# Optimization experiments

Measured on AMD Instinct MI355X. Metric: run time of the kernel, lower is better.

The kernel has to match this reference:

```python
import jax, jax.numpy as jnp
import numpy as np

N_GRAPHS = 256
BN_EPS = 1e-5

def gcn_conv(x, row, col, W, b, n):
    # PyG GCNConv: add self-loops, symmetric deg^-1/2 normalization, scatter-add at col.
    deg = jnp.zeros((n,), x.dtype).at[col].add(1.0) + 1.0  # +1 for self-loop
    dinv = jax.lax.rsqrt(deg)
    xw = x @ W                                             # [N, H]
    msg = (dinv[row] * dinv[col])[:, None] * xw[row]       # [E, H] gathered messages
    agg = jnp.zeros_like(xw).at[col].add(msg)              # scatter-add to targets
    agg = agg + (dinv * dinv)[:, None] * xw                # self-loop contribution
    return agg + b

def batch_norm(x, gamma, beta):
    # BatchNorm1d over the node dimension (training-mode batch statistics)
    mu = jnp.mean(x, axis=0)
    var = jnp.var(x, axis=0)
    return (x - mu) * jax.lax.rsqrt(var + BN_EPS) * gamma + beta

def setup_inputs():
    key = jax.random.key(0)
    ks = jax.random.split(key, 8)
    N, F, H, C, E = 50000, 128, 128, 3, 1_600_000
    x = jax.random.normal(ks[0], (N, F), jnp.float32)
    edge_index = jax.random.randint(ks[1], (2, E), 0, N)
    batch = jnp.sort(jax.random.randint(ks[2], (N,), 0, N_GRAPHS))
    s = lambda k, sh, fan: jax.random.normal(k, sh, jnp.float32) / np.sqrt(fan).astype(np.float32)
    return {
        "x": x, "edge_index": edge_index, "batch": batch,
        "W1": s(ks[3], (F, H), F), "b1": jnp.zeros((H,), jnp.float32),
        "gamma1": jnp.ones((H,), jnp.float32), "beta1": jnp.zeros((H,), jnp.float32),
        "W2": s(ks[4], (H, H), H), "b2": jnp.zeros((H,), jnp.float32),
        "gamma2": jnp.ones((H,), jnp.float32), "beta2": jnp.zeros((H,), jnp.float32),
        "Wc": s(ks[5], (3 * H, C), 3 * H), "bc": jnp.zeros((C,), jnp.float32),
    }

def reference(x, edge_index, batch, W1, b1, gamma1, beta1, W2, b2, gamma2, beta2, Wc, bc):
    n = x.shape[0]
    row, col = edge_index[0], edge_index[1]
    h = jax.nn.relu(batch_norm(gcn_conv(x, row, col, W1, b1, n), gamma1, beta1))
    # dropout is identity in eval mode
    h = jax.nn.relu(batch_norm(gcn_conv(h, row, col, W2, b2, n), gamma2, beta2))
    cnt = jax.ops.segment_sum(jnp.ones((n,), h.dtype), batch, num_segments=N_GRAPHS)
    hsum = jax.ops.segment_sum(h, batch, num_segments=N_GRAPHS)
    hmean = hsum / jnp.maximum(cnt, 1.0)[:, None]
    hmax = jax.ops.segment_max(h, batch, num_segments=N_GRAPHS)
    hmax = jnp.where(cnt[:, None] > 0, hmax, 0.0)  # guard empty graphs
    g = jnp.concatenate([hmean, hmax, hsum], axis=1)  # [G, 3H]
    return g @ Wc + bc
```

## Files before the change

kernel.cpp:

```cpp
#include <hip/hip_runtime.h>

#define HF 128
#define TILE 128
#define CAP2 6144
#define NFINE_MAX 512
#define SORT_CHUNK 2048
#define BN_EPS 1e-5f
#define SMEM_FUSED 22528

__device__ __forceinline__ unsigned short f2bf(float f) {
    unsigned u = __float_as_uint(f);
    unsigned rounding = 0x7FFF + ((u >> 16) & 1);
    return (unsigned short)((u + rounding) >> 16);
}
__device__ __forceinline__ float bf2f(unsigned short u) {
    return __uint_as_float(((unsigned)u) << 16);
}
__device__ __forceinline__ unsigned packbf(float lo, float hi) {
    return ((unsigned)f2bf(hi) << 16) | (unsigned)f2bf(lo);
}

__device__ __forceinline__ void bucket_sort_block(char* smem, int bid,
                                                  const int* __restrict__ row,
                                                  const int* __restrict__ col,
                                                  unsigned* __restrict__ buckets,
                                                  int* __restrict__ cursor,
                                                  int E, int nfine) {
    unsigned* staged = (unsigned*)smem;
    unsigned short* sbkt = (unsigned short*)(smem + 8192);
    int* hist  = (int*)(smem + 12288);
    int* lbase = (int*)(smem + 14336);
    int* gbase = (int*)(smem + 16384);
    int* lofs  = (int*)(smem + 18432);
    int* s     = (int*)(smem + 20480);
    int t = threadIdx.x;
    for (int i = t; i < NFINE_MAX; i += 256) { hist[i] = 0; lofs[i] = 0; }
    __syncthreads();
    int e0 = bid * SORT_CHUNK + t * 8;
    int cc[8], rr[8], pg[8];
    unsigned pk[8];
    if (e0 + 8 <= E) {
        int4 c0 = *reinterpret_cast<const int4*>(col + e0);
        int4 c1 = *reinterpret_cast<const int4*>(col + e0 + 4);
        int4 r0 = *reinterpret_cast<const int4*>(row + e0);
        int4 r1 = *reinterpret_cast<const int4*>(row + e0 + 4);
        cc[0]=c0.x; cc[1]=c0.y; cc[2]=c0.z; cc[3]=c0.w;
        cc[4]=c1.x; cc[5]=c1.y; cc[6]=c1.z; cc[7]=c1.w;
        rr[0]=r0.x; rr[1]=r0.y; rr[2]=r0.z; rr[3]=r0.w;
        rr[4]=r1.x; rr[5]=r1.y; rr[6]=r1.z; rr[7]=r1.w;
    } else {
        #pragma unroll
        for (int i = 0; i < 8; ++i) {
            int e = e0 + i;
            cc[i] = (e < E) ? col[e] : -1;
            rr[i] = (e < E) ? row[e] : 0;
        }
    }
    #pragma unroll
    for (int i = 0; i < 8; ++i) {
        if (cc[i] >= 0) {
            int b = cc[i] >> 7;
            pg[i] = b;
            pk[i] = ((unsigned)(cc[i] & 127) << 17) | (unsigned)rr[i];
            atomicAdd(&hist[b], 1);
        } else {
            pg[i] = -1;
        }
    }
    __syncthreads();
    s[t] = hist[t];
    s[t + 256] = hist[t + 256];
    for (int o = 1; o < 512; o <<= 1) {
        __syncthreads();
        int idx = (t + 1) * (o << 1) - 1;
        if (idx < 512) s[idx] += s[idx - o];
    }
    __syncthreads();
    if (t == 0) s[511] = 0;
    for (int o = 256; o >= 1; o >>= 1) {
        __syncthreads();
        int idx = (t + 1) * (o << 1) - 1;
        if (idx < 512) { int tmp = s[idx - o]; s[idx - o] = s[idx]; s[idx] += tmp; }
    }
    __syncthreads();
    lbase[t] = s[t];
    lbase[t + 256] = s[t + 256];
    for (int b = t; b < nfine; b += 256) {
        int cnt = hist[b];
        gbase[b] = cnt ? atomicAdd(&cursor[b * 16], cnt) : 0;
    }
    __syncthreads();
    #pragma unroll
    for (int i = 0; i < 8; ++i) {
        if (pg[i] >= 0) {
            int pos = lbase[pg[i]] + atomicAdd(&lofs[pg[i]], 1);
            staged[pos] = pk[i];
            sbkt[pos] = (unsigned short)pg[i];
        }
    }
    __syncthreads();
    int n = min(SORT_CHUNK, E - bid * SORT_CHUNK);
    for (int i = t; i < n; i += 256) {
        int b = sbkt[i];
        int pos = gbase[b] + (i - lbase[b]);
        if (pos < CAP2) buckets[(size_t)b * CAP2 + pos] = staged[i];
    }
}

__device__ __forceinline__ void gemm_block32(char* smem, int bid,
                                             const float* __restrict__ X,
                                             const float* __restrict__ W,
                                             unsigned short* __restrict__ Y, int N) {
    float (*xst)[36] = (float(*)[36])smem;
    int t = threadIdx.x;
    int row0 = bid * 32;
    {
        int f = t & 127;
        for (int r = (t >> 7); r < 32; r += 2) {
            int rr = row0 + r;
            xst[f][r] = (rr < N) ? X[(size_t)rr * HF + f] : 0.0f;
        }
    }
    __syncthreads();
    int cg = t & 31;
    int rg = t >> 5;
    int r0 = rg * 4;
    float acc[4][4] = {};
    const float4* Wv = reinterpret_cast<const float4*>(W);
    #pragma unroll 4
    for (int f = 0; f < HF; ++f) {
        float4 w = Wv[f * 32 + cg];
        float4 xv = *reinterpret_cast<const float4*>(&xst[f][r0]);
        float xr[4] = {xv.x, xv.y, xv.z, xv.w};
        #pragma unroll
        for (int i = 0; i < 4; ++i) {
            acc[i][0] += xr[i] * w.x;
            acc[i][1] += xr[i] * w.y;
            acc[i][2] += xr[i] * w.z;
            acc[i][3] += xr[i] * w.w;
        }
    }
    #pragma unroll
    for (int i = 0; i < 4; ++i) {
        int rr = row0 + r0 + i;
        if (rr < N) {
            ushort4 o;
            o.x = f2bf(acc[i][0]);
            o.y = f2bf(acc[i][1]);
            o.z = f2bf(acc[i][2]);
            o.w = f2bf(acc[i][3]);
            *reinterpret_cast<ushort4*>(&Y[(size_t)rr * HF + cg * 4]) = o;
        }
    }
}

__global__ __launch_bounds__(256) void sort_gemm1(const int* __restrict__ row,
                                                  const int* __restrict__ col,
                                                  unsigned* __restrict__ buckets,
                                                  int* __restrict__ cursor,
                                                  int E, int nfine, int nsort,
                                                  const float* __restrict__ x,
                                                  const float* __restrict__ W1,
                                                  unsigned short* __restrict__ A,
                                                  int N) {
    __shared__ __align__(16) char smem[SMEM_FUSED];
    if (blockIdx.x < nsort)
        bucket_sort_block(smem, blockIdx.x, row, col, buckets, cursor, E, nfine);
    else
        gemm_block32(smem, blockIdx.x - nsort, x, W1, A, N);
}

__global__ __launch_bounds__(256) void gemm_rt(const unsigned short* __restrict__ Xh,
                                               const float* __restrict__ W,
                                               unsigned short* __restrict__ Y,
                                               const float* __restrict__ scale,
                                               const float* __restrict__ shift,
                                               const float* __restrict__ rowscale,
                                               int N) {
    __shared__ float xst[HF][68];
    int t = threadIdx.x;
    int row0 = blockIdx.x * 64;
    {
        int f = t & 127;
        float sc = scale[f];
        float sh = shift[f];
        for (int r = (t >> 7); r < 64; r += 2) {
            int rr = row0 + r;
            float v = 0.0f;
            if (rr < N) {
                v = bf2f(Xh[(size_t)rr * HF + f]);
                v = fmaxf(v * sc + sh, 0.0f);
            }
            xst[f][r] = v;
        }
    }
    __syncthreads();
    int cg = t & 31;
    int rg = t >> 5;
    int r0 = rg * 8;
    float acc[8][4] = {};
    const float4* Wv = reinterpret_cast<const float4*>(W);
    #pragma unroll 2
    for (int f = 0; f < HF; ++f) {
        float4 w = Wv[f * 32 + cg];
        float4 x0 = *reinterpret_cast<const float4*>(&xst[f][r0]);
        float4 x1 = *reinterpret_cast<const float4*>(&xst[f][r0 + 4]);
        float xr[8] = {x0.x, x0.y, x0.z, x0.w, x1.x, x1.y, x1.z, x1.w};
        #pragma unroll
        for (int i = 0; i < 8; ++i) {
            acc[i][0] += xr[i] * w.x;
            acc[i][1] += xr[i] * w.y;
            acc[i][2] += xr[i] * w.z;
            acc[i][3] += xr[i] * w.w;
        }
    }
    #pragma unroll
    for (int i = 0; i < 8; ++i) {
        int rr = row0 + r0 + i;
        if (rr < N) {
            float rs = rowscale[rr];
            ushort4 o;
            o.x = f2bf(acc[i][0] * rs);
            o.y = f2bf(acc[i][1] * rs);
            o.z = f2bf(acc[i][2] * rs);
            o.w = f2bf(acc[i][3] * rs);
            *reinterpret_cast<ushort4*>(&Y[(size_t)rr * HF + cg * 4]) = o;
        }
    }
}

__global__ __launch_bounds__(256) void tile_place2(const unsigned* __restrict__ buckets,
                                                   const int* __restrict__ cursor,
                                                   int* __restrict__ rowptr,
                                                   float* __restrict__ dinv,
                                                   int* __restrict__ srow,
                                                   unsigned short* __restrict__ A,
                                                   const int* __restrict__ batch,
                                                   int* __restrict__ gstart,
                                                   int N, int NG, int nfine) {
    int b = blockIdx.x;
    int t = threadIdx.x;
    if (b < 2 && t < 129) {
        int g = b * 129 + t;
        if (g <= NG) {
            int lo = 0, hi = N;
            while (lo < hi) {
                int mid = (lo + hi) >> 1;
                if (batch[mid] < g) lo = mid + 1; else hi = mid;
            }
            gstart[g] = lo;
        }
    }
    __shared__ int h[TILE], loc[TILE], cur[TILE];
    __shared__ float dloc[TILE];
    __shared__ int red[256];
    __shared__ int stage[CAP2];
    int part = 0;
    for (int i = t; i < b; i += 256) part += min(cursor[i * 16], CAP2);
    red[t] = part;
    if (t < TILE) h[t] = 0;
    __syncthreads();
    for (int o = 128; o > 0; o >>= 1) {
        if (t < o) red[t] += red[t + o];
        __syncthreads();
    }
    int base = red[0];
    int sz = min(cursor[b * 16], CAP2);
    const unsigned* bk = buckets + (size_t)b * CAP2;
    for (int i = t; i < sz; i += 256) atomicAdd(&h[bk[i] >> 17], 1);
    __syncthreads();
    if (t < TILE) loc[t] = h[t];
    __syncthreads();
    for (int o = 1; o < TILE; o <<= 1) {
        int v = (t < TILE && t >= o) ? loc[t - o] : 0;
        __syncthreads();
        if (t < TILE) loc[t] += v;
        __syncthreads();
    }
    int c0 = b * TILE;
    int ncols = min(TILE, N - c0);
    if (t < TILE) {
        int c = c0 + t;
        int excl = loc[t] - h[t];
        float dc = rsqrtf((float)h[t] + 1.0f);
        if (c < N) {
            rowptr[c] = base + excl;
            dinv[c] = dc;
        }
        dloc[t] = dc;
        cur[t] = excl;
    }
    if (b == nfine - 1 && t == 0) rowptr[N] = base + sz;
    __syncthreads();
    for (int i = t; i < sz; i += 256) {
        unsigned p = bk[i];
        int pos = atomicAdd(&cur[p >> 17], 1);
        if (pos < CAP2) stage[pos] = (int)(p & 0x1FFFFu);
    }
    __syncthreads();
    for (int i = t; i < sz; i += 256) srow[base + i] = stage[i];
    const unsigned M = 0xffff0000u;
    for (int i = t; i < ncols * 16; i += 256) {
        int nl = i >> 4, j = i & 15;
        float dc = dloc[nl];
        unsigned short* ap = A + (size_t)(c0 + nl) * HF + j * 8;
        uint4 u = *reinterpret_cast<const uint4*>(ap);
        uint4 o;
        o.x = packbf(__uint_as_float(u.x << 16) * dc, __uint_as_float(u.x & M) * dc);
        o.y = packbf(__uint_as_float(u.y << 16) * dc, __uint_as_float(u.y & M) * dc);
        o.z = packbf(__uint_as_float(u.z << 16) * dc, __uint_as_float(u.z & M) * dc);
        o.w = packbf(__uint_as_float(u.w << 16) * dc, __uint_as_float(u.w & M) * dc);
        *reinterpret_cast<uint4*>(ap) = o;
    }
}

__global__ __launch_bounds__(256) void gather_conv(const int* __restrict__ rowptr,
                                                   const int* __restrict__ srow,
                                                   const float* __restrict__ dinv,
                                                   const unsigned short* __restrict__ XW,
                                                   const float* __restrict__ b,
                                                   unsigned short* __restrict__ OUT,
                                                   float* __restrict__ psum,
                                                   float* __restrict__ psq, int N) {
    int blk = blockIdx.x;
    int c = blk * 16 + (threadIdx.x >> 4);
    int j = threadIdx.x & 15;
    bool valid = (c < N);
    const unsigned M = 0xffff0000u;
    float o[8];
    if (valid) {
        int e = rowptr[c], end = rowptr[c + 1];
        float acc[8] = {0.f, 0.f, 0.f, 0.f, 0.f, 0.f, 0.f, 0.f};
        for (; e + 3 < end; e += 4) {
            int r0 = srow[e], r1 = srow[e + 1], r2 = srow[e + 2], r3 = srow[e + 3];
            uint4 u0 = *reinterpret_cast<const uint4*>(XW + (size_t)r0 * HF + j * 8);
            uint4 u1 = *reinterpret_cast<const uint4*>(XW + (size_t)r1 * HF + j * 8);
            uint4 u2 = *reinterpret_cast<const uint4*>(XW + (size_t)r2 * HF + j * 8);
            uint4 u3 = *reinterpret_cast<const uint4*>(XW + (size_t)r3 * HF + j * 8);
            acc[0] += (__uint_as_float(u0.x << 16) + __uint_as_float(u1.x << 16))
                    + (__uint_as_float(u2.x << 16) + __uint_as_float(u3.x << 16));
            acc[1] += (__uint_as_float(u0.x & M) + __uint_as_float(u1.x & M))
                    + (__uint_as_float(u2.x & M) + __uint_as_float(u3.x & M));
            acc[2] += (__uint_as_float(u0.y << 16) + __uint_as_float(u1.y << 16))
                    + (__uint_as_float(u2.y << 16) + __uint_as_float(u3.y << 16));
            acc[3] += (__uint_as_float(u0.y & M) + __uint_as_float(u1.y & M))
                    + (__uint_as_float(u2.y & M) + __uint_as_float(u3.y & M));
            acc[4] += (__uint_as_float(u0.z << 16) + __uint_as_float(u1.z << 16))
                    + (__uint_as_float(u2.z << 16) + __uint_as_float(u3.z << 16));
            acc[5] += (__uint_as_float(u0.z & M) + __uint_as_float(u1.z & M))
                    + (__uint_as_float(u2.z & M) + __uint_as_float(u3.z & M));
            acc[6] += (__uint_as_float(u0.w << 16) + __uint_as_float(u1.w << 16))
                    + (__uint_as_float(u2.w << 16) + __uint_as_float(u3.w << 16));
            acc[7] += (__uint_as_float(u0.w & M) + __uint_as_float(u1.w & M))
                    + (__uint_as_float(u2.w & M) + __uint_as_float(u3.w & M));
        }
        for (; e < end; ++e) {
            int r0 = srow[e];
            uint4 u0 = *reinterpret_cast<const uint4*>(XW + (size_t)r0 * HF + j * 8);
            acc[0] += __uint_as_float(u0.x << 16);
            acc[1] += __uint_as_float(u0.x & M);
            acc[2] += __uint_as_float(u0.y << 16);
            acc[3] += __uint_as_float(u0.y & M);
            acc[4] += __uint_as_float(u0.z << 16);
            acc[5] += __uint_as_float(u0.z & M);
            acc[6] += __uint_as_float(u0.w << 16);
            acc[7] += __uint_as_float(u0.w & M);
        }
        float dc = dinv[c];
        uint4 xv = *reinterpret_cast<const uint4*>(XW + (size_t)c * HF + j * 8);
        acc[0] += __uint_as_float(xv.x << 16);
        acc[1] += __uint_as_float(xv.x & M);
        acc[2] += __uint_as_float(xv.y << 16);
        acc[3] += __uint_as_float(xv.y & M);
        acc[4] += __uint_as_float(xv.z << 16);
        acc[5] += __uint_as_float(xv.z & M);
        acc[6] += __uint_as_float(xv.w << 16);
        acc[7] += __uint_as_float(xv.w & M);
        float4 b0 = *reinterpret_cast<const float4*>(b + j * 8);
        float4 b1 = *reinterpret_cast<const float4*>(b + j * 8 + 4);
        o[0] = dc * acc[0] + b0.x;
        o[1] = dc * acc[1] + b0.y;
        o[2] = dc * acc[2] + b0.z;
        o[3] = dc * acc[3] + b0.w;
        o[4] = dc * acc[4] + b1.x;
        o[5] = dc * acc[5] + b1.y;
        o[6] = dc * acc[6] + b1.z;
        o[7] = dc * acc[7] + b1.w;
        uint4 ov;
        ov.x = packbf(o[0], o[1]);
        ov.y = packbf(o[2], o[3]);
        ov.z = packbf(o[4], o[5]);
        ov.w = packbf(o[6], o[7]);
        *reinterpret_cast<uint4*>(OUT + (size_t)c * HF + j * 8) = ov;
    } else {
        #pragma unroll
        for (int k = 0; k < 8; ++k) o[k] = 0.f;
    }
    __shared__ float sval[16][HF + 4];
    int r = threadIdx.x >> 4;
    *reinterpret_cast<float4*>(&sval[r][j * 8]) = make_float4(o[0], o[1], o[2], o[3]);
    *reinterpret_cast<float4*>(&sval[r][j * 8 + 4]) = make_float4(o[4], o[5], o[6], o[7]);
    __syncthreads();
    if (threadIdx.x < HF) {
        float s = 0.f, sq = 0.f;
        #pragma unroll
        for (int rr = 0; rr < 16; ++rr) {
            float v = sval[rr][threadIdx.x];
            s += v;
            sq += v * v;
        }
        psum[(size_t)blk * HF + threadIdx.x] = s;
        psq[(size_t)blk * HF + threadIdx.x] = sq;
    }
}

__global__ __launch_bounds__(256) void bn_reduce(const float* __restrict__ psum,
                                                 const float* __restrict__ psq,
                                                 const float* __restrict__ gamma,
                                                 const float* __restrict__ beta,
                                                 float* __restrict__ scale,
                                                 float* __restrict__ shift,
                                                 int nblk, int N) {
    int f = blockIdx.x;
    int t = threadIdx.x;
    float s = 0.f, sq = 0.f;
    for (int i = t; i < nblk; i += 256) {
        s += psum[(size_t)i * HF + f];
        sq += psq[(size_t)i * HF + f];
    }
    __shared__ float ls[256], lq[256];
    ls[t] = s; lq[t] = sq;
    __syncthreads();
    for (int o = 128; o > 0; o >>= 1) {
        if (t < o) { ls[t] += ls[t + o]; lq[t] += lq[t + o]; }
        __syncthreads();
    }
    if (t == 0) {
        float invn = 1.0f / (float)N;
        float mu = ls[0] * invn;
        float var = lq[0] * invn - mu * mu;
        float sc = gamma[f] * rsqrtf(var + BN_EPS);
        scale[f] = sc;
        shift[f] = beta[f] - mu * sc;
    }
}

__global__ __launch_bounds__(256) void pool_classify(const unsigned short* __restrict__ Bh,
                                                     const int* __restrict__ gstart,
                                                     const float* __restrict__ scale,
                                                     const float* __restrict__ shift,
                                                     const float* __restrict__ Wc,
                                                     const float* __restrict__ bc,
                                                     float* __restrict__ out) {
    int g = blockIdx.x;
    int t = threadIdx.x & 127;
    int half = threadIdx.x >> 7;
    int s0 = gstart[g], s1 = gstart[g + 1];
    float sc = scale[t], sh = shift[t];
    float sum = 0.f, mx = 0.f;
    for (int n = s0 + half; n < s1; n += 2) {
        float v = fmaxf(bf2f(Bh[(size_t)n * HF + t]) * sc + sh, 0.0f);
        sum += v;
        mx = fmaxf(mx, v);
    }
    __shared__ float shsum[2][HF], shmax[2][HF];
    __shared__ float red[3][HF];
    shsum[half][t] = sum;
    shmax[half][t] = mx;
    __syncthreads();
    if (half == 0) {
        sum += shsum[1][t];
        mx = fmaxf(mx, shmax[1][t]);
        float cntf = (float)(s1 - s0);
        float mean = sum / fmaxf(cntf, 1.0f);
        red[0][t] = mean * Wc[t * 3 + 0] + mx * Wc[(HF + t) * 3 + 0] + sum * Wc[(2 * HF + t) * 3 + 0];
        red[1][t] = mean * Wc[t * 3 + 1] + mx * Wc[(HF + t) * 3 + 1] + sum * Wc[(2 * HF + t) * 3 + 1];
        red[2][t] = mean * Wc[t * 3 + 2] + mx * Wc[(HF + t) * 3 + 2] + sum * Wc[(2 * HF + t) * 3 + 2];
    }
    __syncthreads();
    for (int o = 64; o > 0; o >>= 1) {
        if (half == 0 && t < o) {
            red[0][t] += red[0][t + o];
            red[1][t] += red[1][t + o];
            red[2][t] += red[2][t + o];
        }
        __syncthreads();
    }
    if (threadIdx.x < 3) out[g * 3 + threadIdx.x] = red[threadIdx.x][0] + bc[threadIdx.x];
}

extern "C" void kernel_launch(void* const* d_in, const int* in_sizes, int n_in,
                              void* d_out, int out_size, void* d_ws, size_t ws_size,
                              hipStream_t stream) {
    const float* x    = (const float*)d_in[0];
    const int*   ei   = (const int*)d_in[1];
    const int*   batch= (const int*)d_in[2];
    const float* W1   = (const float*)d_in[3];
    const float* b1   = (const float*)d_in[4];
    const float* g1   = (const float*)d_in[5];
    const float* be1  = (const float*)d_in[6];
    const float* W2   = (const float*)d_in[7];
    const float* b2   = (const float*)d_in[8];
    const float* g2   = (const float*)d_in[9];
    const float* be2  = (const float*)d_in[10];
    const float* Wc   = (const float*)d_in[11];
    const float* bc   = (const float*)d_in[12];
    float* out = (float*)d_out;

    const int N = in_sizes[0] / HF;
    const int E = in_sizes[1] / 2;
    const int NG = 256;
    const int* row = ei;
    const int* col = ei + E;
    const int total = N * HF;
    const int nfine = (N + TILE - 1) / TILE;
    const int nblkGa = (N + 15) / 16;

    char* w = (char*)d_ws;
    size_t off = 0;
    auto alloc = [&](size_t bytes) -> void* {
        void* p = w + off;
        off += (bytes + 255) & ~(size_t)255;
        return p;
    };
    int*            cursor    = (int*)alloc((size_t)nfine * 16 * 4);
    float*          dinv      = (float*)alloc((size_t)N * 4);
    int*            rowptr    = (int*)alloc(((size_t)N + 1) * 4);
    int*            gstart    = (int*)alloc((NG + 1) * 4);
    int*            srow      = (int*)alloc((size_t)E * 4);
    float*          psum      = (float*)alloc((size_t)nblkGa * HF * 4);
    float*          psq       = (float*)alloc((size_t)nblkGa * HF * 4);
    float*          scale     = (float*)alloc(HF * 4);
    float*          shift     = (float*)alloc(HF * 4);
    unsigned short* A         = (unsigned short*)alloc((size_t)total * 2);
    unsigned short* B         = (unsigned short*)alloc((size_t)total * 2);
    unsigned*       buckets   = (unsigned*)B;

    const int T256 = 256;
    int gridGemm64 = (N + 63) / 64;
    int gridGemm32 = (N + 31) / 32;
    int nsort      = (E + SORT_CHUNK - 1) / SORT_CHUNK;

    hipMemsetAsync(cursor, 0, (size_t)nfine * 16 * 4, stream);
    sort_gemm1<<<nsort + gridGemm32, T256, 0, stream>>>(row, col, buckets, cursor,
                                                        E, nfine, nsort, x, W1, A, N);
    tile_place2<<<nfine, T256, 0, stream>>>(buckets, cursor, rowptr, dinv, srow, A,
                                            batch, gstart, N, NG, nfine);

    gather_conv<<<nblkGa, T256, 0, stream>>>(rowptr, srow, dinv, A, b1, B, psum, psq, N);
    bn_reduce<<<HF, 256, 0, stream>>>(psum, psq, g1, be1, scale, shift, nblkGa, N);

    gemm_rt<<<gridGemm64, T256, 0, stream>>>(B, W2, A, scale, shift, dinv, N);
    gather_conv<<<nblkGa, T256, 0, stream>>>(rowptr, srow, dinv, A, b2, B, psum, psq, N);
    bn_reduce<<<HF, 256, 0, stream>>>(psum, psq, g2, be2, scale, shift, nblkGa, N);

    pool_classify<<<NG, 256, 0, stream>>>(B, gstart, scale, shift, Wc, bc, out);
}
```

Measured before the change: 292.8 us.

## Double sort chunk and first-GEMM row tile in fused sort/GEMM kernel

Each bucket-sort block now processes 4096 edges with strided loops that re-read col/row from global memory instead of holding 8 edges per thread in registers. Fewer blocks mean fewer global cursor atomics and longer contiguous runs per bucket. The first GEMM now computes 64 rows per block with 8x4 accumulators per thread, reusing each W load across more rows. Shared memory grows to about 34 KB and register use rises, which may reduce occupancy, and col is now read twice per edge.

```diff
diff --git a/kernel.cpp b/kernel.cpp
--- a/kernel.cpp
+++ b/kernel.cpp
@@ -4,9 +4,9 @@
 #define TILE 128
 #define CAP2 6144
 #define NFINE_MAX 512
-#define SORT_CHUNK 2048
+#define SORT_CHUNK 4096
 #define BN_EPS 1e-5f
-#define SMEM_FUSED 22528
+#define SMEM_BYTES 34816
 
 __device__ __forceinline__ unsigned short f2bf(float f) {
     unsigned u = __float_as_uint(f);
@@ -27,45 +27,20 @@
                                                   int* __restrict__ cursor,
                                                   int E, int nfine) {
     unsigned* staged = (unsigned*)smem;
-    unsigned short* sbkt = (unsigned short*)(smem + 8192);
-    int* hist  = (int*)(smem + 12288);
-    int* lbase = (int*)(smem + 14336);
-    int* gbase = (int*)(smem + 16384);
-    int* lofs  = (int*)(smem + 18432);
-    int* s     = (int*)(smem + 20480);
+    unsigned short* sbkt = (unsigned short*)(smem + 16384);
+    int* hist  = (int*)(smem + 24576);
+    int* lbase = (int*)(smem + 26624);
+    int* gbase = (int*)(smem + 28672);
+    int* lofs  = (int*)(smem + 30720);
+    int* s     = (int*)(smem + 32768);
     int t = threadIdx.x;
     for (int i = t; i < NFINE_MAX; i += 256) { hist[i] = 0; lofs[i] = 0; }
     __syncthreads();
-    int e0 = bid * SORT_CHUNK + t * 8;
-    int cc[8], rr[8], pg[8];
-    unsigned pk[8];
-    if (e0 + 8 <= E) {
-        int4 c0 = *reinterpret_cast<const int4*>(col + e0);
-        int4 c1 = *reinterpret_cast<const int4*>(col + e0 + 4);
-        int4 r0 = *reinterpret_cast<const int4*>(row + e0);
-        int4 r1 = *reinterpret_cast<const int4*>(row + e0 + 4);
-        cc[0]=c0.x; cc[1]=c0.y; cc[2]=c0.z; cc[3]=c0.w;
-        cc[4]=c1.x; cc[5]=c1.y; cc[6]=c1.z; cc[7]=c1.w;
-        rr[0]=r0.x; rr[1]=r0.y; rr[2]=r0.z; rr[3]=r0.w;
-        rr[4]=r1.x; rr[5]=r1.y; rr[6]=r1.z; rr[7]=r1.w;
-    } else {
-        #pragma unroll
-        for (int i = 0; i < 8; ++i) {
-            int e = e0 + i;
-            cc[i] = (e < E) ? col[e] : -1;
-            rr[i] = (e < E) ? row[e] : 0;
-        }
-    }
-    #pragma unroll
-    for (int i = 0; i < 8; ++i) {
-        if (cc[i] >= 0) {
-            int b = cc[i] >> 7;
-            pg[i] = b;
-            pk[i] = ((unsigned)(cc[i] & 127) << 17) | (unsigned)rr[i];
-            atomicAdd(&hist[b], 1);
-        } else {
-            pg[i] = -1;
-        }
+    int e0 = bid * SORT_CHUNK;
+    int n = min(SORT_CHUNK, E - e0);
+    for (int i = t; i < n; i += 256) {
+        int c = col[e0 + i];
+        atomicAdd(&hist[c >> 7], 1);
     }
     __syncthreads();
     s[t] = hist[t];
@@ -90,16 +65,15 @@
         gbase[b] = cnt ? atomicAdd(&cursor[b * 16], cnt) : 0;
     }
     __syncthreads();
-    #pragma unroll
-    for (int i = 0; i < 8; ++i) {
-        if (pg[i] >= 0) {
-            int pos = lbase[pg[i]] + atomicAdd(&lofs[pg[i]], 1);
-            staged[pos] = pk[i];
-            sbkt[pos] = (unsigned short)pg[i];
-        }
-    }
-    __syncthreads();
-    int n = min(SORT_CHUNK, E - bid * SORT_CHUNK);
+    for (int i = t; i < n; i += 256) {
+        int c = col[e0 + i];
+        int r = row[e0 + i];
+        int b = c >> 7;
+        int pos = lbase[b] + atomicAdd(&lofs[b], 1);
+        staged[pos] = ((unsigned)(c & 127) << 17) | (unsigned)r;
+        sbkt[pos] = (unsigned short)b;
+    }
+    __syncthreads();
     for (int i = t; i < n; i += 256) {
         int b = sbkt[i];
         int pos = gbase[b] + (i - lbase[b]);
@@ -107,16 +81,16 @@
     }
 }
 
-__device__ __forceinline__ void gemm_block32(char* smem, int bid,
+__device__ __forceinline__ void gemm_block64(char* smem, int bid,
                                              const float* __restrict__ X,
                                              const float* __restrict__ W,
                                              unsigned short* __restrict__ Y, int N) {
-    float (*xst)[36] = (float(*)[36])smem;
+    float (*xst)[68] = (float(*)[68])smem;
     int t = threadIdx.x;
-    int row0 = bid * 32;
+    int row0 = bid * 64;
     {
         int f = t & 127;
-        for (int r = (t >> 7); r < 32; r += 2) {
+        for (int r = (t >> 7); r < 64; r += 2) {
             int rr = row0 + r;
             xst[f][r] = (rr < N) ? X[(size_t)rr * HF + f] : 0.0f;
         }
@@ -124,16 +98,17 @@
     __syncthreads();
     int cg = t & 31;
     int rg = t >> 5;
-    int r0 = rg * 4;
-    float acc[4][4] = {};
+    int r0 = rg * 8;
+    float acc[8][4] = {};
     const float4* Wv = reinterpret_cast<const float4*>(W);
-    #pragma unroll 4
+    #pragma unroll 2
     for (int f = 0; f < HF; ++f) {
         float4 w = Wv[f * 32 + cg];
-        float4 xv = *reinterpret_cast<const float4*>(&xst[f][r0]);
-        float xr[4] = {xv.x, xv.y, xv.z, xv.w};
+        float4 x0 = *reinterpret_cast<const float4*>(&xst[f][r0]);
+        float4 x1 = *reinterpret_cast<const float4*>(&xst[f][r0 + 4]);
+        float xr[8] = {x0.x, x0.y, x0.z, x0.w, x1.x, x1.y, x1.z, x1.w};
         #pragma unroll
-        for (int i = 0; i < 4; ++i) {
+        for (int i = 0; i < 8; ++i) {
             acc[i][0] += xr[i] * w.x;
             acc[i][1] += xr[i] * w.y;
             acc[i][2] += xr[i] * w.z;
@@ -141,7 +116,7 @@
         }
     }
     #pragma unroll
-    for (int i = 0; i < 4; ++i) {
+    for (int i = 0; i < 8; ++i) {
         int rr = row0 + r0 + i;
         if (rr < N) {
             ushort4 o;
@@ -163,11 +138,11 @@
                                                   const float* __restrict__ W1,
                                                   unsigned short* __restrict__ A,
                                                   int N) {
-    __shared__ __align__(16) char smem[SMEM_FUSED];
+    __shared__ __align__(16) char smem[SMEM_BYTES];
     if (blockIdx.x < nsort)
         bucket_sort_block(smem, blockIdx.x, row, col, buckets, cursor, E, nfine);
     else
-        gemm_block32(smem, blockIdx.x - nsort, x, W1, A, N);
+        gemm_block64(smem, blockIdx.x - nsort, x, W1, A, N);
 }
 
 __global__ __launch_bounds__(256) void gemm_rt(const unsigned short* __restrict__ Xh,
@@ -538,11 +513,10 @@
 
     const int T256 = 256;
     int gridGemm64 = (N + 63) / 64;
-    int gridGemm32 = (N + 31) / 32;
     int nsort      = (E + SORT_CHUNK - 1) / SORT_CHUNK;
 
     hipMemsetAsync(cursor, 0, (size_t)nfine * 16 * 4, stream);
-    sort_gemm1<<<nsort + gridGemm32, T256, 0, stream>>>(row, col, buckets, cursor,
+    sort_gemm1<<<nsort + gridGemm64, T256, 0, stream>>>(row, col, buckets, cursor,
                                                         E, nfine, nsort, x, W1, A, N);
     tile_place2<<<nfine, T256, 0, stream>>>(buckets, cursor, rowptr, dinv, srow, A,
                                             batch, gstart, N, NG, nfine);
```

New measurement: 281.4 us. -3.9%, faster.
